# Kernel tuning notes

Measured on AMD Instinct MI355X. Metric: run time of the kernel, lower is better.

## Reference

```python
import jax, jax.numpy as jnp
import numpy as np

NUM_HEADS = 16
D_MODEL = 1024
D_KV = 64
NUM_BUCKETS = 32
MAX_DISTANCE = 128


def _relative_position_bucket(relative_position, num_buckets=NUM_BUCKETS, max_distance=MAX_DISTANCE):
    # faithful port of the torch static method (bidirectional variant)
    n = -relative_position
    nb = num_buckets // 2
    ret = (n < 0).astype(jnp.int32) * nb
    n = jnp.abs(n)
    max_exact = nb // 2
    is_small = n < max_exact
    # guard log(0); is_small branch covers n < max_exact anyway
    val_if_large = max_exact + (
        jnp.log(jnp.maximum(n, 1).astype(jnp.float32) / max_exact)
        / np.log(max_distance / max_exact)
        * (nb - max_exact)
    ).astype(jnp.int32)
    val_if_large = jnp.minimum(val_if_large, nb - 1)
    return ret + jnp.where(is_small, n, val_if_large)


def _compute_bias(seq_len, rel_bias):
    ctx = jnp.arange(seq_len)[:, None]
    mem = jnp.arange(seq_len)[None, :]
    bucket = _relative_position_bucket(mem - ctx)  # [S, S]
    values = rel_bias[bucket]                      # [S, S, H]
    return jnp.transpose(values, (2, 0, 1))[None]  # [1, H, S, S]


def setup_inputs() -> dict:
    key = jax.random.key(0)
    ks = jax.random.split(key, 6)
    B, S = 4, 1024
    scale = 1.0 / np.sqrt(D_MODEL)
    return {
        "hidden_states": jax.random.normal(ks[0], (B, S, D_MODEL), jnp.float32),
        "attention_mask": jnp.ones((B, 1, 1, S), jnp.int32),
        "Wq": jax.random.normal(ks[1], (NUM_HEADS * D_KV, D_MODEL), jnp.float32) * scale,
        "Wk": jax.random.normal(ks[2], (NUM_HEADS * D_KV, D_MODEL), jnp.float32) * scale,
        "Wv": jax.random.normal(ks[3], (NUM_HEADS * D_KV, D_MODEL), jnp.float32) * scale,
        "Wo": jax.random.normal(ks[4], (D_MODEL, NUM_HEADS * D_KV), jnp.float32) * scale,
        "rel_bias": jax.random.normal(ks[5], (NUM_BUCKETS, NUM_HEADS), jnp.float32),
    }


def reference(hidden_states, attention_mask, Wq, Wk, Wv, Wo, rel_bias):
    B, S, _ = hidden_states.shape
    # projections (Linear with bias=False: x @ W.T), reshape to [B, S, H, d_kv]
    q = jnp.einsum('bsd,ed->bse', hidden_states, Wq).reshape(B, S, NUM_HEADS, D_KV)
    k = jnp.einsum('bsd,ed->bse', hidden_states, Wk).reshape(B, S, NUM_HEADS, D_KV)
    v = jnp.einsum('bsd,ed->bse', hidden_states, Wv).reshape(B, S, NUM_HEADS, D_KV)
    scores = jnp.einsum('bqhd,bkhd->bhqk', q, k) / np.sqrt(D_KV)
    scores = scores + _compute_bias(S, rel_bias)
    scores = jnp.where(attention_mask == 0, jnp.float32(-1e9), scores)
    attn_weights = jax.nn.softmax(scores, axis=-1)  # dropout is identity at eval
    attn_output = jnp.einsum('bhqk,bkhd->bqhd', attn_weights, v).reshape(B, S, NUM_HEADS * D_KV)
    output = jnp.einsum('bse,de->bsd', attn_output, Wo)
    return output, attn_weights
```

## Files before the change

kernel.cpp:

```cpp
#include <hip/hip_runtime.h>
#include <hip/hip_bf16.h>

#define BB 4
#define SS 1024
#define HH 16
#define DK 64
#define DM 1024
#define MM (BB * SS)

typedef __attribute__((ext_vector_type(8))) short bh8_t;
typedef __attribute__((ext_vector_type(4))) float f4_t;

#define MFMA(a, b, c) __builtin_amdgcn_mfma_f32_16x16x32_bf16(a, b, c, 0, 0, 0)

__device__ __forceinline__ short f2bf(float f) {
    unsigned u = __builtin_bit_cast(unsigned, f);
    u = (u + 0x7FFFu + ((u >> 16) & 1u)) >> 16;
    return (short)u;
}
__device__ __forceinline__ float bf2f(short h) {
    unsigned u = ((unsigned)(unsigned short)h) << 16;
    return __builtin_bit_cast(float, u);
}

__device__ __forceinline__ int rel_bucket(int rel) {
    int n = -rel;
    int ret = 0;
    if (n < 0) { ret = 16; n = -n; }
    int v;
    if (n < 8) {
        v = n;
    } else {
        float t = logf((float)n * 0.125f) / 2.7725887298583984f * 8.0f;
        v = 8 + (int)t;
        if (v > 15) v = 15;
    }
    return ret + v;
}

__global__ __launch_bounds__(256)
void k_proj_qk(const float* __restrict__ X, const float* __restrict__ Wq,
               const float* __restrict__ Wk,
               short* __restrict__ Qh, short* __restrict__ Ql,
               short* __restrict__ Kh, short* __restrict__ Kl) {
    const int z = blockIdx.z;
    const float* W = z ? Wk : Wq;
    short* Oh = z ? Kh : Qh;
    short* Ol = z ? Kl : Ql;

    __shared__ short Ah[128][40], Al[128][40], Bh[128][40], Bl[128][40];

    const int tid = threadIdx.x;
    const int m0 = blockIdx.y * 128, n0 = blockIdx.x * 128;
    const int wave = tid >> 6, lane = tid & 63;
    const int quad = lane >> 4, lm = lane & 15;
    const int wm = (wave >> 1) * 64, wn = (wave & 1) * 64;
    const int r = tid >> 1, sg = (tid & 1) * 16;

    f4_t acc[4][4];
#pragma unroll
    for (int i = 0; i < 4; ++i)
#pragma unroll
        for (int j = 0; j < 4; ++j) acc[i][j] = (f4_t){0.f, 0.f, 0.f, 0.f};

    for (int k0 = 0; k0 < DM; k0 += 32) {
        f4_t xa[4], wb[4];
#pragma unroll
        for (int u = 0; u < 4; ++u) {
            xa[u] = *(const f4_t*)(X + (size_t)(m0 + r) * DM + k0 + sg + u * 4);
            wb[u] = *(const f4_t*)(W + (size_t)(n0 + r) * DM + k0 + sg + u * 4);
        }
        __syncthreads();
#pragma unroll
        for (int u = 0; u < 4; ++u) {
            short4 hh, ll;
            hh.x = f2bf(xa[u][0]); ll.x = f2bf(xa[u][0] - bf2f(hh.x));
            hh.y = f2bf(xa[u][1]); ll.y = f2bf(xa[u][1] - bf2f(hh.y));
            hh.z = f2bf(xa[u][2]); ll.z = f2bf(xa[u][2] - bf2f(hh.z));
            hh.w = f2bf(xa[u][3]); ll.w = f2bf(xa[u][3] - bf2f(hh.w));
            *(short4*)&Ah[r][sg + u * 4] = hh;
            *(short4*)&Al[r][sg + u * 4] = ll;
            hh.x = f2bf(wb[u][0]); ll.x = f2bf(wb[u][0] - bf2f(hh.x));
            hh.y = f2bf(wb[u][1]); ll.y = f2bf(wb[u][1] - bf2f(hh.y));
            hh.z = f2bf(wb[u][2]); ll.z = f2bf(wb[u][2] - bf2f(hh.z));
            hh.w = f2bf(wb[u][3]); ll.w = f2bf(wb[u][3] - bf2f(hh.w));
            *(short4*)&Bh[r][sg + u * 4] = hh;
            *(short4*)&Bl[r][sg + u * 4] = ll;
        }
        __syncthreads();

        bh8_t ah[4], al[4];
#pragma unroll
        for (int i = 0; i < 4; ++i) {
            ah[i] = *(const bh8_t*)&Ah[wm + i * 16 + lm][quad * 8];
            al[i] = *(const bh8_t*)&Al[wm + i * 16 + lm][quad * 8];
        }
#pragma unroll
        for (int j = 0; j < 4; ++j) {
            bh8_t bhj = *(const bh8_t*)&Bh[wn + j * 16 + lm][quad * 8];
            bh8_t blj = *(const bh8_t*)&Bl[wn + j * 16 + lm][quad * 8];
#pragma unroll
            for (int i = 0; i < 4; ++i) {
                acc[i][j] = MFMA(al[i], bhj, acc[i][j]);
                acc[i][j] = MFMA(ah[i], blj, acc[i][j]);
                acc[i][j] = MFMA(ah[i], bhj, acc[i][j]);
            }
        }
    }

#pragma unroll
    for (int i = 0; i < 4; ++i)
#pragma unroll
        for (int j = 0; j < 4; ++j)
#pragma unroll
            for (int g = 0; g < 4; ++g) {
                const int row = m0 + wm + i * 16 + quad * 4 + g;
                const int col = n0 + wn + j * 16 + lm;
                const int b = row >> 10, s = row & 1023;
                const int hd = col >> 6, dk = col & 63;
                const float v = acc[i][j][g];
                const short vh = f2bf(v);
                const short vl = f2bf(v - bf2f(vh));
                const size_t o = ((size_t)((b * HH + hd) * SS + s)) * DK + dk;
                Oh[o] = vh;
                Ol[o] = vl;
            }
}

__global__ __launch_bounds__(256)
void k_proj_v(const float* __restrict__ X, const float* __restrict__ Wv,
              short* __restrict__ Vt) {
    __shared__ short As[128][40], Bs[128][40];

    const int tid = threadIdx.x;
    const int m0 = blockIdx.y * 128, n0 = blockIdx.x * 128;
    const int wave = tid >> 6, lane = tid & 63;
    const int quad = lane >> 4, lm = lane & 15;
    const int wm = (wave >> 1) * 64, wn = (wave & 1) * 64;
    const int r = tid >> 1, sg = (tid & 1) * 16;

    f4_t acc[4][4];
#pragma unroll
    for (int i = 0; i < 4; ++i)
#pragma unroll
        for (int j = 0; j < 4; ++j) acc[i][j] = (f4_t){0.f, 0.f, 0.f, 0.f};

    for (int k0 = 0; k0 < DM; k0 += 32) {
        f4_t xa[4], wb[4];
#pragma unroll
        for (int u = 0; u < 4; ++u) {
            xa[u] = *(const f4_t*)(X + (size_t)(m0 + r) * DM + k0 + sg + u * 4);
            wb[u] = *(const f4_t*)(Wv + (size_t)(n0 + r) * DM + k0 + sg + u * 4);
        }
        __syncthreads();
#pragma unroll
        for (int u = 0; u < 4; ++u) {
            short4 hh;
            hh.x = f2bf(xa[u][0]); hh.y = f2bf(xa[u][1]);
            hh.z = f2bf(xa[u][2]); hh.w = f2bf(xa[u][3]);
            *(short4*)&As[r][sg + u * 4] = hh;
            hh.x = f2bf(wb[u][0]); hh.y = f2bf(wb[u][1]);
            hh.z = f2bf(wb[u][2]); hh.w = f2bf(wb[u][3]);
            *(short4*)&Bs[r][sg + u * 4] = hh;
        }
        __syncthreads();

        bh8_t ah[4];
#pragma unroll
        for (int i = 0; i < 4; ++i)
            ah[i] = *(const bh8_t*)&As[wm + i * 16 + lm][quad * 8];
#pragma unroll
        for (int j = 0; j < 4; ++j) {
            bh8_t bhj = *(const bh8_t*)&Bs[wn + j * 16 + lm][quad * 8];
#pragma unroll
            for (int i = 0; i < 4; ++i) acc[i][j] = MFMA(ah[i], bhj, acc[i][j]);
        }
    }

#pragma unroll
    for (int i = 0; i < 4; ++i)
#pragma unroll
        for (int j = 0; j < 4; ++j)
#pragma unroll
            for (int g = 0; g < 4; ++g) {
                const int row = m0 + wm + i * 16 + quad * 4 + g;
                const int col = n0 + wn + j * 16 + lm;
                const int b = row >> 10, s = row & 1023;
                const int hd = col >> 6, dk = col & 63;
                Vt[((size_t)((b * HH + hd) * DK + dk)) * SS + s] = f2bf(acc[i][j][g]);
            }
}

#define EPAD 1044

__global__ __launch_bounds__(256)
void k_fused(const short* __restrict__ Qh, const short* __restrict__ Ql,
             const short* __restrict__ Kh, const short* __restrict__ Kl,
             const short* __restrict__ Vt, const int* __restrict__ mask,
             const float* __restrict__ rb, float* __restrict__ P,
             short* __restrict__ AO) {
    __shared__ __align__(16) char smem[75328];
    float* E     = (float*)smem;
    float* redS  = (float*)smem;
    float* biasS = (float*)(smem + 66816);
    int*   maskS = (int*)(smem + 70976);
    float* wmaxS = (float*)(smem + 75072);

    const int tid = threadIdx.x;
    const int bid = blockIdx.x;
    const int swz = (bid & 7) * 512 + (bid >> 3);
    const int qb = swz & 63, bh = swz >> 6;
    const int b = bh >> 4, hd = bh & 15;
    const int q0 = qb * 16;
    const int wave = tid >> 6, lane = tid & 63;
    const int quad = lane >> 4, lm = lane & 15;

    for (int i = tid; i < 1040; i += 256)
        biasS[i] = rb[rel_bucket(i - q0 - 15) * HH + hd];
    for (int i = tid; i < 1024; i += 256) maskS[i] = mask[b * SS + i];

    bh8_t qah[2], qal[2];
#pragma unroll
    for (int ks = 0; ks < 2; ++ks) {
        const size_t qo = ((size_t)bh * SS + q0 + lm) * DK + ks * 32 + quad * 8;
        qah[ks] = *(const bh8_t*)(Qh + qo);
        qal[ks] = *(const bh8_t*)(Ql + qo);
    }
    __syncthreads();

    float pmax[4] = {-3.0e38f, -3.0e38f, -3.0e38f, -3.0e38f};

    for (int kt = 0; kt < 8; ++kt) {
        const int kb = kt * 128 + wave * 32;
        f4_t acc[2];
        acc[0] = (f4_t){0.f, 0.f, 0.f, 0.f};
        acc[1] = (f4_t){0.f, 0.f, 0.f, 0.f};
        bh8_t kh[2][2], kl[2][2];
#pragma unroll
        for (int j = 0; j < 2; ++j)
#pragma unroll
            for (int ks = 0; ks < 2; ++ks) {
                const size_t ko =
                    ((size_t)bh * SS + kb + j * 16 + lm) * DK + ks * 32 + quad * 8;
                kh[j][ks] = *(const bh8_t*)(Kh + ko);
                kl[j][ks] = *(const bh8_t*)(Kl + ko);
            }
#pragma unroll
        for (int j = 0; j < 2; ++j)
#pragma unroll
            for (int ks = 0; ks < 2; ++ks) {
                acc[j] = MFMA(qal[ks], kh[j][ks], acc[j]);
                acc[j] = MFMA(qah[ks], kl[j][ks], acc[j]);
                acc[j] = MFMA(qah[ks], kh[j][ks], acc[j]);
            }
#pragma unroll
        for (int j = 0; j < 2; ++j) {
            const int col = kb + j * 16 + lm;
            const int msk = maskS[col];
#pragma unroll
            for (int g = 0; g < 4; ++g) {
                const int rl = quad * 4 + g;
                float s = acc[j][g] * 0.125f + biasS[col - rl + 15];
                s = (msk == 0) ? -1e9f : s;
                E[rl * EPAD + col] = s;
                pmax[g] = fmaxf(pmax[g], s);
            }
        }
    }
#pragma unroll
    for (int g = 0; g < 4; ++g) {
        float m = pmax[g];
        m = fmaxf(m, __shfl_xor(m, 1, 64));
        m = fmaxf(m, __shfl_xor(m, 2, 64));
        m = fmaxf(m, __shfl_xor(m, 4, 64));
        m = fmaxf(m, __shfl_xor(m, 8, 64));
        if (lm == 0) wmaxS[wave * 16 + quad * 4 + g] = m;
    }
    __syncthreads();

    {
        const int row = tid >> 4;
        const int cc = (tid & 15) * 4;
        const float m = fmaxf(fmaxf(wmaxS[row], wmaxS[16 + row]),
                              fmaxf(wmaxS[32 + row], wmaxS[48 + row]));
        f4_t ev[16];
        float sum = 0.f;
#pragma unroll
        for (int u = 0; u < 16; ++u) {
            f4_t s4 = *(const f4_t*)&E[row * EPAD + cc + u * 64];
            f4_t e;
            e[0] = expf(s4[0] - m);
            e[1] = expf(s4[1] - m);
            e[2] = expf(s4[2] - m);
            e[3] = expf(s4[3] - m);
            ev[u] = e;
            sum += e[0] + e[1] + e[2] + e[3];
        }
        sum += __shfl_xor(sum, 1, 64);
        sum += __shfl_xor(sum, 2, 64);
        sum += __shfl_xor(sum, 4, 64);
        sum += __shfl_xor(sum, 8, 64);
        const float inv = 1.0f / sum;
        float* Pr = P + ((size_t)bh * SS + q0 + row) * SS;
#pragma unroll
        for (int u = 0; u < 16; ++u) {
            f4_t p;
            p[0] = ev[u][0] * inv;
            p[1] = ev[u][1] * inv;
            p[2] = ev[u][2] * inv;
            p[3] = ev[u][3] * inv;
            *(f4_t*)&E[row * EPAD + cc + u * 64] = p;
            *(f4_t*)(Pr + cc + u * 64) = p;
        }
    }
    __syncthreads();

    f4_t acc[4];
#pragma unroll
    for (int f = 0; f < 4; ++f) acc[f] = (f4_t){0.f, 0.f, 0.f, 0.f};

    for (int kk = 0; kk < 8; ++kk) {
        const int kg = wave * 256 + kk * 32 + quad * 8;
        f4_t p0 = *(const f4_t*)&E[lm * EPAD + kg];
        f4_t p1 = *(const f4_t*)&E[lm * EPAD + kg + 4];
        bh8_t pa;
        pa[0] = f2bf(p0[0]); pa[1] = f2bf(p0[1]);
        pa[2] = f2bf(p0[2]); pa[3] = f2bf(p0[3]);
        pa[4] = f2bf(p1[0]); pa[5] = f2bf(p1[1]);
        pa[6] = f2bf(p1[2]); pa[7] = f2bf(p1[3]);
#pragma unroll
        for (int f = 0; f < 4; ++f) {
            bh8_t vb =
                *(const bh8_t*)(Vt + ((size_t)bh * DK + f * 16 + lm) * SS + kg);
            acc[f] = MFMA(pa, vb, acc[f]);
        }
    }
    __syncthreads();
#pragma unroll
    for (int f = 0; f < 4; ++f)
#pragma unroll
        for (int g = 0; g < 4; ++g)
            redS[((size_t)wave * 16 + quad * 4 + g) * 64 + f * 16 + lm] = acc[f][g];
    __syncthreads();

    {
        const int flat = tid * 4;
        const int q = flat >> 6, dk = flat & 63;
        f4_t s0 = *(const f4_t*)&redS[(0 * 16 + q) * 64 + dk];
        f4_t s1 = *(const f4_t*)&redS[(1 * 16 + q) * 64 + dk];
        f4_t s2 = *(const f4_t*)&redS[(2 * 16 + q) * 64 + dk];
        f4_t s3 = *(const f4_t*)&redS[(3 * 16 + q) * 64 + dk];
        short4 o;
        o.x = f2bf(s0[0] + s1[0] + s2[0] + s3[0]);
        o.y = f2bf(s0[1] + s1[1] + s2[1] + s3[1]);
        o.z = f2bf(s0[2] + s1[2] + s2[2] + s3[2]);
        o.w = f2bf(s0[3] + s1[3] + s2[3] + s3[3]);
        *(short4*)(AO + ((size_t)(b * SS + q0 + q)) * DM + hd * DK + dk) = o;
    }
}

__global__ __launch_bounds__(256)
void k_out(const short* __restrict__ A, const float* __restrict__ Wo,
           float* __restrict__ Out) {
    __shared__ short As[128][40], Bs[128][40];

    const int tid = threadIdx.x;
    const int m0 = blockIdx.y * 128, n0 = blockIdx.x * 128;
    const int wave = tid >> 6, lane = tid & 63;
    const int quad = lane >> 4, lm = lane & 15;
    const int wm = (wave >> 1) * 64, wn = (wave & 1) * 64;
    const int r = tid >> 1, sg = (tid & 1) * 16;

    f4_t acc[4][4];
#pragma unroll
    for (int i = 0; i < 4; ++i)
#pragma unroll
        for (int j = 0; j < 4; ++j) acc[i][j] = (f4_t){0.f, 0.f, 0.f, 0.f};

    for (int k0 = 0; k0 < DM; k0 += 32) {
        uint4 a0 = *(const uint4*)(A + (size_t)(m0 + r) * DM + k0 + sg);
        uint4 a1 = *(const uint4*)(A + (size_t)(m0 + r) * DM + k0 + sg + 8);
        f4_t wb[4];
#pragma unroll
        for (int u = 0; u < 4; ++u)
            wb[u] = *(const f4_t*)(Wo + (size_t)(n0 + r) * DM + k0 + sg + u * 4);
        __syncthreads();
        *(uint4*)&As[r][sg] = a0;
        *(uint4*)&As[r][sg + 8] = a1;
#pragma unroll
        for (int u = 0; u < 4; ++u) {
            short4 hh;
            hh.x = f2bf(wb[u][0]); hh.y = f2bf(wb[u][1]);
            hh.z = f2bf(wb[u][2]); hh.w = f2bf(wb[u][3]);
            *(short4*)&Bs[r][sg + u * 4] = hh;
        }
        __syncthreads();

        bh8_t ah[4];
#pragma unroll
        for (int i = 0; i < 4; ++i)
            ah[i] = *(const bh8_t*)&As[wm + i * 16 + lm][quad * 8];
#pragma unroll
        for (int j = 0; j < 4; ++j) {
            bh8_t bhj = *(const bh8_t*)&Bs[wn + j * 16 + lm][quad * 8];
#pragma unroll
            for (int i = 0; i < 4; ++i) acc[i][j] = MFMA(ah[i], bhj, acc[i][j]);
        }
    }

#pragma unroll
    for (int i = 0; i < 4; ++i)
#pragma unroll
        for (int j = 0; j < 4; ++j)
#pragma unroll
            for (int g = 0; g < 4; ++g)
                Out[(size_t)(m0 + wm + i * 16 + quad * 4 + g) * DM + n0 + wn + j * 16 + lm] =
                    acc[i][j][g];
}

extern "C" void kernel_launch(void* const* d_in, const int* in_sizes, int n_in,
                              void* d_out, int out_size, void* d_ws, size_t ws_size,
                              hipStream_t stream) {
    const float* X    = (const float*)d_in[0];
    const int*   mask = (const int*)d_in[1];
    const float* Wq   = (const float*)d_in[2];
    const float* Wk   = (const float*)d_in[3];
    const float* Wv   = (const float*)d_in[4];
    const float* Wo   = (const float*)d_in[5];
    const float* rb   = (const float*)d_in[6];

    float* out = (float*)d_out;
    float* P   = out + (size_t)BB * SS * DM;

    short* ws = (short*)d_ws;
    short* Qh = ws;
    short* Ql = ws + (size_t)4194304;
    short* Kh = ws + (size_t)8388608;
    short* Kl = ws + (size_t)12582912;
    short* Vt = ws + (size_t)16777216;
    short* AO = ws + (size_t)20971520;

    k_proj_qk<<<dim3(8, 32, 2), 256, 0, stream>>>(X, Wq, Wk, Qh, Ql, Kh, Kl);
    k_proj_v <<<dim3(8, 32, 1), 256, 0, stream>>>(X, Wv, Vt);
    k_fused  <<<dim3(4096), 256, 0, stream>>>(Qh, Ql, Kh, Kl, Vt, mask, rb, P, AO);
    k_out    <<<dim3(8, 32), 256, 0, stream>>>(AO, Wo, out);
}
```

Measured before the change: 646.8 us.

## Merge QKV projection kernels and widen fused attention block to 512 threads

Combines the Q/K and V projection kernels into one launch using blockIdx.z to select the path, removing a kernel launch and letting V blocks run alongside Q/K blocks. The fused attention kernel now uses 8 waves per 16-row query tile instead of 4, so each wave handles fewer key columns. The softmax, PV product and cross-wave reduction are reindexed to match, and expf is replaced by the faster __expf. This trades more parallelism per block for a larger 8-way reduction and higher register and LDS pressure per block.

New measurement: 645.5 us. Within noise of the previous version (-0.2%).

```diff
diff --git a/kernel.cpp b/kernel.cpp
--- a/kernel.cpp
+++ b/kernel.cpp
@@ -39,14 +39,12 @@
 }
 
 __global__ __launch_bounds__(256)
-void k_proj_qk(const float* __restrict__ X, const float* __restrict__ Wq,
-               const float* __restrict__ Wk,
-               short* __restrict__ Qh, short* __restrict__ Ql,
-               short* __restrict__ Kh, short* __restrict__ Kl) {
+void k_proj(const float* __restrict__ X, const float* __restrict__ Wq,
+            const float* __restrict__ Wk, const float* __restrict__ Wv,
+            short* __restrict__ Qh, short* __restrict__ Ql,
+            short* __restrict__ Kh, short* __restrict__ Kl,
+            short* __restrict__ Vt) {
     const int z = blockIdx.z;
-    const float* W = z ? Wk : Wq;
-    short* Oh = z ? Kh : Qh;
-    short* Ol = z ? Kl : Ql;
 
     __shared__ short Ah[128][40], Al[128][40], Bh[128][40], Bl[128][40];
 
@@ -63,143 +61,130 @@
 #pragma unroll
         for (int j = 0; j < 4; ++j) acc[i][j] = (f4_t){0.f, 0.f, 0.f, 0.f};
 
-    for (int k0 = 0; k0 < DM; k0 += 32) {
-        f4_t xa[4], wb[4];
-#pragma unroll
-        for (int u = 0; u < 4; ++u) {
-            xa[u] = *(const f4_t*)(X + (size_t)(m0 + r) * DM + k0 + sg + u * 4);
-            wb[u] = *(const f4_t*)(W + (size_t)(n0 + r) * DM + k0 + sg + u * 4);
-        }
-        __syncthreads();
-#pragma unroll
-        for (int u = 0; u < 4; ++u) {
-            short4 hh, ll;
-            hh.x = f2bf(xa[u][0]); ll.x = f2bf(xa[u][0] - bf2f(hh.x));
-            hh.y = f2bf(xa[u][1]); ll.y = f2bf(xa[u][1] - bf2f(hh.y));
-            hh.z = f2bf(xa[u][2]); ll.z = f2bf(xa[u][2] - bf2f(hh.z));
-            hh.w = f2bf(xa[u][3]); ll.w = f2bf(xa[u][3] - bf2f(hh.w));
-            *(short4*)&Ah[r][sg + u * 4] = hh;
-            *(short4*)&Al[r][sg + u * 4] = ll;
-            hh.x = f2bf(wb[u][0]); ll.x = f2bf(wb[u][0] - bf2f(hh.x));
-            hh.y = f2bf(wb[u][1]); ll.y = f2bf(wb[u][1] - bf2f(hh.y));
-            hh.z = f2bf(wb[u][2]); ll.z = f2bf(wb[u][2] - bf2f(hh.z));
-            hh.w = f2bf(wb[u][3]); ll.w = f2bf(wb[u][3] - bf2f(hh.w));
-            *(short4*)&Bh[r][sg + u * 4] = hh;
-            *(short4*)&Bl[r][sg + u * 4] = ll;
-        }
-        __syncthreads();
-
-        bh8_t ah[4], al[4];
-#pragma unroll
-        for (int i = 0; i < 4; ++i) {
-            ah[i] = *(const bh8_t*)&Ah[wm + i * 16 + lm][quad * 8];
-            al[i] = *(const bh8_t*)&Al[wm + i * 16 + lm][quad * 8];
-        }
-#pragma unroll
-        for (int j = 0; j < 4; ++j) {
-            bh8_t bhj = *(const bh8_t*)&Bh[wn + j * 16 + lm][quad * 8];
-            bh8_t blj = *(const bh8_t*)&Bl[wn + j * 16 + lm][quad * 8];
+    if (z < 2) {
+        const float* W = z ? Wk : Wq;
+        short* Oh = z ? Kh : Qh;
+        short* Ol = z ? Kl : Ql;
+
+        for (int k0 = 0; k0 < DM; k0 += 32) {
+            f4_t xa[4], wb[4];
+#pragma unroll
+            for (int u = 0; u < 4; ++u) {
+                xa[u] = *(const f4_t*)(X + (size_t)(m0 + r) * DM + k0 + sg + u * 4);
+                wb[u] = *(const f4_t*)(W + (size_t)(n0 + r) * DM + k0 + sg + u * 4);
+            }
+            __syncthreads();
+#pragma unroll
+            for (int u = 0; u < 4; ++u) {
+                short4 hh, ll;
+                hh.x = f2bf(xa[u][0]); ll.x = f2bf(xa[u][0] - bf2f(hh.x));
+                hh.y = f2bf(xa[u][1]); ll.y = f2bf(xa[u][1] - bf2f(hh.y));
+                hh.z = f2bf(xa[u][2]); ll.z = f2bf(xa[u][2] - bf2f(hh.z));
+                hh.w = f2bf(xa[u][3]); ll.w = f2bf(xa[u][3] - bf2f(hh.w));
+                *(short4*)&Ah[r][sg + u * 4] = hh;
+                *(short4*)&Al[r][sg + u * 4] = ll;
+                hh.x = f2bf(wb[u][0]); ll.x = f2bf(wb[u][0] - bf2f(hh.x));
+                hh.y = f2bf(wb[u][1]); ll.y = f2bf(wb[u][1] - bf2f(hh.y));
+                hh.z = f2bf(wb[u][2]); ll.z = f2bf(wb[u][2] - bf2f(hh.z));
+                hh.w = f2bf(wb[u][3]); ll.w = f2bf(wb[u][3] - bf2f(hh.w));
+                *(short4*)&Bh[r][sg + u * 4] = hh;
+                *(short4*)&Bl[r][sg + u * 4] = ll;
+            }
+            __syncthreads();
+
+            bh8_t ah[4], al[4];
 #pragma unroll
             for (int i = 0; i < 4; ++i) {
-                acc[i][j] = MFMA(al[i], bhj, acc[i][j]);
-                acc[i][j] = MFMA(ah[i], blj, acc[i][j]);
-                acc[i][j] = MFMA(ah[i], bhj, acc[i][j]);
-            }
-        }
-    }
-
-#pragma unroll
-    for (int i = 0; i < 4; ++i)
-#pragma unroll
-        for (int j = 0; j < 4; ++j)
-#pragma unroll
-            for (int g = 0; g < 4; ++g) {
-                const int row = m0 + wm + i * 16 + quad * 4 + g;
-                const int col = n0 + wn + j * 16 + lm;
-                const int b = row >> 10, s = row & 1023;
-                const int hd = col >> 6, dk = col & 63;
-                const float v = acc[i][j][g];
-                const short vh = f2bf(v);
-                const short vl = f2bf(v - bf2f(vh));
-                const size_t o = ((size_t)((b * HH + hd) * SS + s)) * DK + dk;
-                Oh[o] = vh;
-                Ol[o] = vl;
-            }
-}
-
-__global__ __launch_bounds__(256)
-void k_proj_v(const float* __restrict__ X, const float* __restrict__ Wv,
-              short* __restrict__ Vt) {
-    __shared__ short As[128][40], Bs[128][40];
-
-    const int tid = threadIdx.x;
-    const int m0 = blockIdx.y * 128, n0 = blockIdx.x * 128;
-    const int wave = tid >> 6, lane = tid & 63;
-    const int quad = lane >> 4, lm = lane & 15;
-    const int wm = (wave >> 1) * 64, wn = (wave & 1) * 64;
-    const int r = tid >> 1, sg = (tid & 1) * 16;
-
-    f4_t acc[4][4];
-#pragma unroll
-    for (int i = 0; i < 4; ++i)
-#pragma unroll
-        for (int j = 0; j < 4; ++j) acc[i][j] = (f4_t){0.f, 0.f, 0.f, 0.f};
-
-    for (int k0 = 0; k0 < DM; k0 += 32) {
-        f4_t xa[4], wb[4];
-#pragma unroll
-        for (int u = 0; u < 4; ++u) {
-            xa[u] = *(const f4_t*)(X + (size_t)(m0 + r) * DM + k0 + sg + u * 4);
-            wb[u] = *(const f4_t*)(Wv + (size_t)(n0 + r) * DM + k0 + sg + u * 4);
-        }
-        __syncthreads();
-#pragma unroll
-        for (int u = 0; u < 4; ++u) {
-            short4 hh;
-            hh.x = f2bf(xa[u][0]); hh.y = f2bf(xa[u][1]);
-            hh.z = f2bf(xa[u][2]); hh.w = f2bf(xa[u][3]);
-            *(short4*)&As[r][sg + u * 4] = hh;
-            hh.x = f2bf(wb[u][0]); hh.y = f2bf(wb[u][1]);
-            hh.z = f2bf(wb[u][2]); hh.w = f2bf(wb[u][3]);
-            *(short4*)&Bs[r][sg + u * 4] = hh;
-        }
-        __syncthreads();
-
-        bh8_t ah[4];
+                ah[i] = *(const bh8_t*)&Ah[wm + i * 16 + lm][quad * 8];
+                al[i] = *(const bh8_t*)&Al[wm + i * 16 + lm][quad * 8];
+            }
+#pragma unroll
+            for (int j = 0; j < 4; ++j) {
+                bh8_t bhj = *(const bh8_t*)&Bh[wn + j * 16 + lm][quad * 8];
+                bh8_t blj = *(const bh8_t*)&Bl[wn + j * 16 + lm][quad * 8];
+#pragma unroll
+                for (int i = 0; i < 4; ++i) {
+                    acc[i][j] = MFMA(al[i], bhj, acc[i][j]);
+                    acc[i][j] = MFMA(ah[i], blj, acc[i][j]);
+                    acc[i][j] = MFMA(ah[i], bhj, acc[i][j]);
+                }
+            }
+        }
+
 #pragma unroll
         for (int i = 0; i < 4; ++i)
-            ah[i] = *(const bh8_t*)&As[wm + i * 16 + lm][quad * 8];
-#pragma unroll
-        for (int j = 0; j < 4; ++j) {
-            bh8_t bhj = *(const bh8_t*)&Bs[wn + j * 16 + lm][quad * 8];
-#pragma unroll
-            for (int i = 0; i < 4; ++i) acc[i][j] = MFMA(ah[i], bhj, acc[i][j]);
-        }
-    }
-
-#pragma unroll
-    for (int i = 0; i < 4; ++i)
-#pragma unroll
-        for (int j = 0; j < 4; ++j)
-#pragma unroll
-            for (int g = 0; g < 4; ++g) {
-                const int row = m0 + wm + i * 16 + quad * 4 + g;
-                const int col = n0 + wn + j * 16 + lm;
-                const int b = row >> 10, s = row & 1023;
-                const int hd = col >> 6, dk = col & 63;
-                Vt[((size_t)((b * HH + hd) * DK + dk)) * SS + s] = f2bf(acc[i][j][g]);
-            }
+#pragma unroll
+            for (int j = 0; j < 4; ++j)
+#pragma unroll
+                for (int g = 0; g < 4; ++g) {
+                    const int row = m0 + wm + i * 16 + quad * 4 + g;
+                    const int col = n0 + wn + j * 16 + lm;
+                    const int b = row >> 10, s = row & 1023;
+                    const int hd = col >> 6, dk = col & 63;
+                    const float v = acc[i][j][g];
+                    const short vh = f2bf(v);
+                    const short vl = f2bf(v - bf2f(vh));
+                    const size_t o = ((size_t)((b * HH + hd) * SS + s)) * DK + dk;
+                    Oh[o] = vh;
+                    Ol[o] = vl;
+                }
+    } else {
+        for (int k0 = 0; k0 < DM; k0 += 32) {
+            f4_t xa[4], wb[4];
+#pragma unroll
+            for (int u = 0; u < 4; ++u) {
+                xa[u] = *(const f4_t*)(X + (size_t)(m0 + r) * DM + k0 + sg + u * 4);
+                wb[u] = *(const f4_t*)(Wv + (size_t)(n0 + r) * DM + k0 + sg + u * 4);
+            }
+            __syncthreads();
+#pragma unroll
+            for (int u = 0; u < 4; ++u) {
+                short4 hh;
+                hh.x = f2bf(xa[u][0]); hh.y = f2bf(xa[u][1]);
+                hh.z = f2bf(xa[u][2]); hh.w = f2bf(xa[u][3]);
+                *(short4*)&Ah[r][sg + u * 4] = hh;
+                hh.x = f2bf(wb[u][0]); hh.y = f2bf(wb[u][1]);
+                hh.z = f2bf(wb[u][2]); hh.w = f2bf(wb[u][3]);
+                *(short4*)&Bh[r][sg + u * 4] = hh;
+            }
+            __syncthreads();
+
+            bh8_t ah[4];
+#pragma unroll
+            for (int i = 0; i < 4; ++i)
+                ah[i] = *(const bh8_t*)&Ah[wm + i * 16 + lm][quad * 8];
+#pragma unroll
+            for (int j = 0; j < 4; ++j) {
+                bh8_t bhj = *(const bh8_t*)&Bh[wn + j * 16 + lm][quad * 8];
+#pragma unroll
+                for (int i = 0; i < 4; ++i) acc[i][j] = MFMA(ah[i], bhj, acc[i][j]);
+            }
+        }
+
+#pragma unroll
+        for (int i = 0; i < 4; ++i)
+#pragma unroll
+            for (int j = 0; j < 4; ++j)
+#pragma unroll
+                for (int g = 0; g < 4; ++g) {
+                    const int row = m0 + wm + i * 16 + quad * 4 + g;
+                    const int col = n0 + wn + j * 16 + lm;
+                    const int b = row >> 10, s = row & 1023;
+                    const int hd = col >> 6, dk = col & 63;
+                    Vt[((size_t)((b * HH + hd) * DK + dk)) * SS + s] = f2bf(acc[i][j][g]);
+                }
+    }
 }
 
 #define EPAD 1044
 
-__global__ __launch_bounds__(256)
+__global__ __launch_bounds__(512, 4)
 void k_fused(const short* __restrict__ Qh, const short* __restrict__ Ql,
              const short* __restrict__ Kh, const short* __restrict__ Kl,
              const short* __restrict__ Vt, const int* __restrict__ mask,
              const float* __restrict__ rb, float* __restrict__ P,
              short* __restrict__ AO) {
-    __shared__ __align__(16) char smem[75328];
+    __shared__ __align__(16) char smem[75584];
     float* E     = (float*)smem;
     float* redS  = (float*)smem;
     float* biasS = (float*)(smem + 66816);
@@ -215,9 +200,9 @@
     const int wave = tid >> 6, lane = tid & 63;
     const int quad = lane >> 4, lm = lane & 15;
 
-    for (int i = tid; i < 1040; i += 256)
+    for (int i = tid; i < 1040; i += 512)
         biasS[i] = rb[rel_bucket(i - q0 - 15) * HH + hd];
-    for (int i = tid; i < 1024; i += 256) maskS[i] = mask[b * SS + i];
+    for (int i = tid; i < 1024; i += 512) maskS[i] = mask[b * SS + i];
 
     bh8_t qah[2], qal[2];
 #pragma unroll
@@ -230,8 +215,9 @@
 
     float pmax[4] = {-3.0e38f, -3.0e38f, -3.0e38f, -3.0e38f};
 
-    for (int kt = 0; kt < 8; ++kt) {
-        const int kb = kt * 128 + wave * 32;
+#pragma unroll
+    for (int kt = 0; kt < 4; ++kt) {
+        const int kb = wave * 128 + kt * 32;
         f4_t acc[2];
         acc[0] = (f4_t){0.f, 0.f, 0.f, 0.f};
         acc[1] = (f4_t){0.f, 0.f, 0.f, 0.f};
@@ -279,20 +265,21 @@
     __syncthreads();
 
     {
-        const int row = tid >> 4;
-        const int cc = (tid & 15) * 4;
-        const float m = fmaxf(fmaxf(wmaxS[row], wmaxS[16 + row]),
-                              fmaxf(wmaxS[32 + row], wmaxS[48 + row]));
-        f4_t ev[16];
+        const int row = tid >> 5;
+        const int cc = (tid & 31) * 4;
+        float m = wmaxS[row];
+#pragma unroll
+        for (int w = 1; w < 8; ++w) m = fmaxf(m, wmaxS[w * 16 + row]);
+        f4_t ev[8];
         float sum = 0.f;
 #pragma unroll
-        for (int u = 0; u < 16; ++u) {
-            f4_t s4 = *(const f4_t*)&E[row * EPAD + cc + u * 64];
+        for (int u = 0; u < 8; ++u) {
+            f4_t s4 = *(const f4_t*)&E[row * EPAD + cc + u * 128];
             f4_t e;
-            e[0] = expf(s4[0] - m);
-            e[1] = expf(s4[1] - m);
-            e[2] = expf(s4[2] - m);
-            e[3] = expf(s4[3] - m);
+            e[0] = __expf(s4[0] - m);
+            e[1] = __expf(s4[1] - m);
+            e[2] = __expf(s4[2] - m);
+            e[3] = __expf(s4[3] - m);
             ev[u] = e;
             sum += e[0] + e[1] + e[2] + e[3];
         }
@@ -300,17 +287,18 @@
         sum += __shfl_xor(sum, 2, 64);
         sum += __shfl_xor(sum, 4, 64);
         sum += __shfl_xor(sum, 8, 64);
+        sum += __shfl_xor(sum, 16, 64);
         const float inv = 1.0f / sum;
         float* Pr = P + ((size_t)bh * SS + q0 + row) * SS;
 #pragma unroll
-        for (int u = 0; u < 16; ++u) {
+        for (int u = 0; u < 8; ++u) {
             f4_t p;
             p[0] = ev[u][0] * inv;
             p[1] = ev[u][1] * inv;
             p[2] = ev[u][2] * inv;
             p[3] = ev[u][3] * inv;
-            *(f4_t*)&E[row * EPAD + cc + u * 64] = p;
-            *(f4_t*)(Pr + cc + u * 64) = p;
+            *(f4_t*)&E[row * EPAD + cc + u * 128] = p;
+            *(f4_t*)(Pr + cc + u * 128) = p;
         }
     }
     __syncthreads();
@@ -319,8 +307,9 @@
 #pragma unroll
     for (int f = 0; f < 4; ++f) acc[f] = (f4_t){0.f, 0.f, 0.f, 0.f};
 
-    for (int kk = 0; kk < 8; ++kk) {
-        const int kg = wave * 256 + kk * 32 + quad * 8;
+#pragma unroll
+    for (int kk = 0; kk < 4; ++kk) {
+        const int kg = wave * 128 + kk * 32 + quad * 8;
         f4_t p0 = *(const f4_t*)&E[lm * EPAD + kg];
         f4_t p1 = *(const f4_t*)&E[lm * EPAD + kg + 4];
         bh8_t pa;
@@ -344,18 +333,18 @@
     __syncthreads();
 
     {
-        const int flat = tid * 4;
+        const int flat = tid * 2;
         const int q = flat >> 6, dk = flat & 63;
-        f4_t s0 = *(const f4_t*)&redS[(0 * 16 + q) * 64 + dk];
-        f4_t s1 = *(const f4_t*)&redS[(1 * 16 + q) * 64 + dk];
-        f4_t s2 = *(const f4_t*)&redS[(2 * 16 + q) * 64 + dk];
-        f4_t s3 = *(const f4_t*)&redS[(3 * 16 + q) * 64 + dk];
-        short4 o;
-        o.x = f2bf(s0[0] + s1[0] + s2[0] + s3[0]);
-        o.y = f2bf(s0[1] + s1[1] + s2[1] + s3[1]);
-        o.z = f2bf(s0[2] + s1[2] + s2[2] + s3[2]);
-        o.w = f2bf(s0[3] + s1[3] + s2[3] + s3[3]);
-        *(short4*)(AO + ((size_t)(b * SS + q0 + q)) * DM + hd * DK + dk) = o;
+        float s0 = 0.f, s1 = 0.f;
+#pragma unroll
+        for (int w = 0; w < 8; ++w) {
+            s0 += redS[((size_t)w * 16 + q) * 64 + dk];
+            s1 += redS[((size_t)w * 16 + q) * 64 + dk + 1];
+        }
+        short2 o;
+        o.x = f2bf(s0);
+        o.y = f2bf(s1);
+        *(short2*)(AO + ((size_t)(b * SS + q0 + q)) * DM + hd * DK + dk) = o;
     }
 }
 
@@ -440,8 +429,7 @@
     short* Vt = ws + (size_t)16777216;
     short* AO = ws + (size_t)20971520;
 
-    k_proj_qk<<<dim3(8, 32, 2), 256, 0, stream>>>(X, Wq, Wk, Qh, Ql, Kh, Kl);
-    k_proj_v <<<dim3(8, 32, 1), 256, 0, stream>>>(X, Wv, Vt);
-    k_fused  <<<dim3(4096), 256, 0, stream>>>(Qh, Ql, Kh, Kl, Vt, mask, rb, P, AO);
-    k_out    <<<dim3(8, 32), 256, 0, stream>>>(AO, Wo, out);
-}
+    k_proj <<<dim3(8, 32, 3), 256, 0, stream>>>(X, Wq, Wk, Wv, Qh, Ql, Kh, Kl, Vt);
+    k_fused<<<dim3(4096), 512, 0, stream>>>(Qh, Ql, Kh, Kl, Vt, mask, rb, P, AO);
+    k_out  <<<dim3(8, 32), 256, 0, stream>>>(AO, Wo, out);
+}
```
